# Kernel tuning notes

Measured on AMD Instinct MI355X. Metric: run time of the kernel, lower is better.

## Reference

```python
import jax, jax.numpy as jnp
import numpy as np

N_NODES = 100000
N_EDGES = 1600000
F_NODE = 32
F_EDGE = 32
HID = 64
N_TGT = 32


def setup_inputs() -> dict:
    key = jax.random.key(0)
    ks = jax.random.split(key, 12)
    x = jax.random.normal(ks[0], (N_NODES, F_NODE), dtype=jnp.float32)
    edge_index = jax.random.randint(ks[1], (2, N_EDGES), 0, N_NODES, dtype=jnp.int64)
    edge_attr = jax.random.normal(ks[2], (N_EDGES, F_EDGE), dtype=jnp.float32)
    u = jax.random.normal(ks[3], (1, 8), dtype=jnp.float32)
    batch = jnp.zeros((N_NODES,), dtype=jnp.int64)
    s1 = 1.0 / np.sqrt(F_NODE + F_EDGE)
    s2 = 1.0 / np.sqrt(HID)
    s3 = 1.0 / np.sqrt(HID + F_NODE)
    W1a = jax.random.uniform(ks[4], (F_NODE + F_EDGE, HID), jnp.float32, -s1, s1)
    b1a = jax.random.uniform(ks[5], (HID,), jnp.float32, -s1, s1)
    W1b = jax.random.uniform(ks[6], (HID, HID), jnp.float32, -s2, s2)
    b1b = jax.random.uniform(ks[7], (HID,), jnp.float32, -s2, s2)
    W2a = jax.random.uniform(ks[8], (HID + F_NODE, HID), jnp.float32, -s3, s3)
    b2a = jax.random.uniform(ks[9], (HID,), jnp.float32, -s3, s3)
    W2b = jax.random.uniform(ks[10], (HID, N_TGT), jnp.float32, -s2, s2)
    b2b = jax.random.uniform(ks[11], (N_TGT,), jnp.float32, -s2, s2)
    return {"x": x, "edge_index": edge_index, "edge_attr": edge_attr, "u": u,
            "batch": batch, "W1a": W1a, "b1a": b1a, "W1b": W1b, "b1b": b1b,
            "W2a": W2a, "b2a": b2a, "W2b": W2b, "b2b": b2b}


def reference(x, edge_index, edge_attr, u, batch,
              W1a, b1a, W1b, b1b, W2a, b2a, W2b, b2b):
    row, col = edge_index[0], edge_index[1]
    n = x.shape[0]
    # gather source node features and concat with edge features -> edge MLP
    m = jnp.concatenate([x[col], edge_attr], axis=1)           # [E, F_NODE+F_EDGE]
    m = jax.nn.relu(m @ W1a + b1a) @ W1b + b1b                  # [E, HID]
    # scatter-mean back to destination nodes (row)
    summed = jax.ops.segment_sum(m, row, num_segments=n)        # [N, HID]
    counts = jax.ops.segment_sum(jnp.ones((m.shape[0],), m.dtype), row, num_segments=n)
    agg = summed / jnp.maximum(counts, 1.0)[:, None]
    h = jnp.concatenate([x, agg], axis=1)                       # [N, HID+F_NODE]
    out = jax.nn.relu(h @ W2a + b2a) @ W2b + b2b                # [N, N_TGT]
    return out
```

## Files before the change

kernel.cpp:

```cpp
#include <hip/hip_runtime.h>

#define NN 100000
#define NE 1600000
#define NB ((NN + 255) / 256)
#define TPW 8

typedef unsigned int uint32;
typedef unsigned short ushort16;
typedef float f32x4 __attribute__((ext_vector_type(4)));
typedef short bf16x8 __attribute__((ext_vector_type(8)));

__device__ __forceinline__ float bflo(uint32 u) { return __uint_as_float(u << 16); }
__device__ __forceinline__ float bfhi(uint32 u) { return __uint_as_float(u & 0xffff0000u); }
__device__ __forceinline__ uint32 bfbits(float v) { return (__float_as_uint(v) + 0x8000u) >> 16; }
__device__ __forceinline__ uint32 pack2(float a, float b) { return bfbits(a) | (bfbits(b) << 16); }

__device__ __forceinline__ int sigma_ch(int c) {
    return (((c >> 2) & 3) << 4) + (((c >> 4) & 3) << 2) + (c & 3);
}

__global__ __launch_bounds__(256) void k_hist_rank(const int* __restrict__ ei, int* __restrict__ deg,
                                                   int* __restrict__ pos, int E) {
    int e = blockIdx.x * 256 + threadIdx.x;
    if (e < E) pos[e] = atomicAdd(&deg[ei[e]], 1);
}

__global__ __launch_bounds__(256) void k_hist(const int* __restrict__ ei, int* __restrict__ deg, int E) {
    int e = blockIdx.x * 256 + threadIdx.x;
    if (e < E) atomicAdd(&deg[ei[e]], 1);
}

__global__ __launch_bounds__(256) void k_scan1(const int* __restrict__ deg, int* __restrict__ offs,
                                               int* __restrict__ bsums, int n) {
    __shared__ int s[256];
    int tid = threadIdx.x;
    int i = blockIdx.x * 256 + tid;
    int v = (i < n) ? deg[i] : 0;
    int acc = v;
    s[tid] = acc;
    __syncthreads();
    #pragma unroll
    for (int off = 1; off < 256; off <<= 1) {
        int t = (tid >= off) ? s[tid - off] : 0;
        __syncthreads();
        acc += t;
        s[tid] = acc;
        __syncthreads();
    }
    if (i < n) offs[i] = acc - v;
    if (tid == 255) bsums[blockIdx.x] = acc;
}

__global__ __launch_bounds__(512) void k_scan2(int* __restrict__ bsums, int nb) {
    __shared__ int s[512];
    int tid = threadIdx.x;
    int v = (tid < nb) ? bsums[tid] : 0;
    int acc = v;
    s[tid] = acc;
    __syncthreads();
    #pragma unroll
    for (int off = 1; off < 512; off <<= 1) {
        int t = (tid >= off) ? s[tid - off] : 0;
        __syncthreads();
        acc += t;
        s[tid] = acc;
        __syncthreads();
    }
    bsums[tid] = acc - v;
}

__global__ __launch_bounds__(256) void k_pos(const int* __restrict__ ei, const int* __restrict__ offs,
                                             const int* __restrict__ bsums, int* __restrict__ pos, int E) {
    int e = blockIdx.x * 256 + threadIdx.x;
    if (e >= E) return;
    int r = ei[e];
    pos[e] += offs[r] + bsums[r >> 8];
}

__global__ __launch_bounds__(256) void k_prep(const float* __restrict__ W1b, const float* __restrict__ b1b,
                                              const float* __restrict__ W2a,
                                              float* __restrict__ Wc, float* __restrict__ bc, int perm) {
    int t = blockIdx.x * 256 + threadIdx.x;
    int r = t >> 6, c = t & 63;
    float a = 0.f;
    for (int k = 0; k < 64; ++k) a += W1b[r * 64 + k] * W2a[(32 + k) * 64 + c];
    int rs = perm ? sigma_ch(r) : r;
    Wc[rs * 64 + c] = a;
    if (t < 64) {
        float bacc = 0.f;
        for (int k = 0; k < 64; ++k) bacc += b1b[k] * W2a[(32 + k) * 64 + t];
        bc[t] = bacc;
    }
}

__global__ __launch_bounds__(256) void k_xa(const float* __restrict__ x, const float* __restrict__ W1a,
                                            const float* __restrict__ b1a, uint32* __restrict__ xa, int N) {
    __shared__ float sW[32 * 64];
    __shared__ float sb[64];
    for (int t = threadIdx.x; t < 32 * 64; t += 256) sW[t] = W1a[t];
    if (threadIdx.x < 64) sb[threadIdx.x] = b1a[threadIdx.x];
    __syncthreads();
    int i = blockIdx.x * 256 + threadIdx.x;
    if (i >= N) return;
    float h[64];
    #pragma unroll
    for (int j = 0; j < 64; ++j) h[j] = sb[j];
    const float4* xrow = (const float4*)(x + (size_t)i * 32);
    #pragma unroll
    for (int k4 = 0; k4 < 8; ++k4) {
        float4 v = xrow[k4];
        float vv[4] = {v.x, v.y, v.z, v.w};
        #pragma unroll
        for (int c = 0; c < 4; ++c) {
            const float4* wr = (const float4*)&sW[(k4 * 4 + c) * 64];
            float val = vv[c];
            #pragma unroll
            for (int j4 = 0; j4 < 16; ++j4) {
                float4 w = wr[j4];
                h[j4 * 4 + 0] += val * w.x; h[j4 * 4 + 1] += val * w.y;
                h[j4 * 4 + 2] += val * w.z; h[j4 * 4 + 3] += val * w.w;
            }
        }
    }
    uint32* xap = xa + (size_t)i * 32;
    #pragma unroll
    for (int q = 0; q < 4; ++q) {
        uint4 t0, t1;
        t0.x = pack2(h[0 * 16 + q * 4 + 0], h[0 * 16 + q * 4 + 1]);
        t0.y = pack2(h[0 * 16 + q * 4 + 2], h[0 * 16 + q * 4 + 3]);
        t0.z = pack2(h[1 * 16 + q * 4 + 0], h[1 * 16 + q * 4 + 1]);
        t0.w = pack2(h[1 * 16 + q * 4 + 2], h[1 * 16 + q * 4 + 3]);
        t1.x = pack2(h[2 * 16 + q * 4 + 0], h[2 * 16 + q * 4 + 1]);
        t1.y = pack2(h[2 * 16 + q * 4 + 2], h[2 * 16 + q * 4 + 3]);
        t1.z = pack2(h[3 * 16 + q * 4 + 0], h[3 * 16 + q * 4 + 1]);
        t1.w = pack2(h[3 * 16 + q * 4 + 2], h[3 * 16 + q * 4 + 3]);
        *(uint4*)(xap + q * 8) = t0;
        *(uint4*)(xap + q * 8 + 4) = t1;
    }
}

__global__ __launch_bounds__(256) void k_edge_mfma(
    const int* __restrict__ ei, const float* __restrict__ ea, const uint32* __restrict__ xa,
    const float* __restrict__ W1a, const int* __restrict__ pos, uint32* __restrict__ g)
{
    __shared__ ushort16 sWt[64 * 40];
    for (int idx = threadIdx.x; idx < 2048; idx += 256) {
        int ch = idx & 63, k = idx >> 6;
        sWt[ch * 40 + k] = (ushort16)bfbits(W1a[(32 + k) * 64 + ch]);
    }
    __syncthreads();

    int lane = threadIdx.x & 63;
    int wave = threadIdx.x >> 6;
    int en = lane & 15;
    int qq = lane >> 4;

    bf16x8 bfr[4];
    #pragma unroll
    for (int cc = 0; cc < 4; ++cc)
        bfr[cc] = *(const bf16x8*)&sWt[(cc * 16 + en) * 40 + qq * 8];

    int base = blockIdx.x * (64 * TPW) + wave * (16 * TPW);

    int e0 = base + en;
    int c0 = ei[NE + e0];
    int p0 = pos[e0];
    float4 f0a = *(const float4*)(ea + (size_t)e0 * 32 + qq * 8);
    float4 f0b = *(const float4*)(ea + (size_t)e0 * 32 + qq * 8 + 4);

    int e1 = base + 16 + en;
    int c1 = ei[NE + e1];
    int p1 = pos[e1];
    float4 f1a = *(const float4*)(ea + (size_t)e1 * 32 + qq * 8);
    float4 f1b = *(const float4*)(ea + (size_t)e1 * 32 + qq * 8 + 4);

    uint4 xv0a = *(const uint4*)(xa + (size_t)c0 * 32 + qq * 8);
    uint4 xv0b = *(const uint4*)(xa + (size_t)c0 * 32 + qq * 8 + 4);

    #pragma unroll 1
    for (int t = 0; t < TPW; ++t) {
        int e2 = base + (t + 2) * 16 + en;
        if (e2 > NE - 1) e2 = NE - 1;
        int c2 = ei[NE + e2];
        int p2 = pos[e2];
        float4 f2a = *(const float4*)(ea + (size_t)e2 * 32 + qq * 8);
        float4 f2b = *(const float4*)(ea + (size_t)e2 * 32 + qq * 8 + 4);
        uint4 xv1a = *(const uint4*)(xa + (size_t)c1 * 32 + qq * 8);
        uint4 xv1b = *(const uint4*)(xa + (size_t)c1 * 32 + qq * 8 + 4);

        union { uint4 u; bf16x8 v; } bf;
        bf.u.x = pack2(f0a.x, f0a.y);
        bf.u.y = pack2(f0a.z, f0a.w);
        bf.u.z = pack2(f0b.x, f0b.y);
        bf.u.w = pack2(f0b.z, f0b.w);

        f32x4 acc[4];
        acc[0] = (f32x4){bflo(xv0a.x), bfhi(xv0a.x), bflo(xv0a.y), bfhi(xv0a.y)};
        acc[1] = (f32x4){bflo(xv0a.z), bfhi(xv0a.z), bflo(xv0a.w), bfhi(xv0a.w)};
        acc[2] = (f32x4){bflo(xv0b.x), bfhi(xv0b.x), bflo(xv0b.y), bfhi(xv0b.y)};
        acc[3] = (f32x4){bflo(xv0b.z), bfhi(xv0b.z), bflo(xv0b.w), bfhi(xv0b.w)};

        #pragma unroll
        for (int cc = 0; cc < 4; ++cc)
            acc[cc] = __builtin_amdgcn_mfma_f32_16x16x32_bf16(bfr[cc], bf.v, acc[cc], 0, 0, 0);

        uint4 o0, o1;
        o0.x = pack2(fmaxf(acc[0][0], 0.f), fmaxf(acc[0][1], 0.f));
        o0.y = pack2(fmaxf(acc[0][2], 0.f), fmaxf(acc[0][3], 0.f));
        o0.z = pack2(fmaxf(acc[1][0], 0.f), fmaxf(acc[1][1], 0.f));
        o0.w = pack2(fmaxf(acc[1][2], 0.f), fmaxf(acc[1][3], 0.f));
        o1.x = pack2(fmaxf(acc[2][0], 0.f), fmaxf(acc[2][1], 0.f));
        o1.y = pack2(fmaxf(acc[2][2], 0.f), fmaxf(acc[2][3], 0.f));
        o1.z = pack2(fmaxf(acc[3][0], 0.f), fmaxf(acc[3][1], 0.f));
        o1.w = pack2(fmaxf(acc[3][2], 0.f), fmaxf(acc[3][3], 0.f));
        uint4* gp = (uint4*)(g + (size_t)p0 * 32 + qq * 8);
        gp[0] = o0;
        gp[1] = o1;

        c0 = c1; p0 = p1; f0a = f1a; f0b = f1b;
        xv0a = xv1a; xv0b = xv1b;
        c1 = c2; p1 = p2; f1a = f2a; f1b = f2b;
    }
}

__global__ __launch_bounds__(256) void k_seg_c(
    const int* __restrict__ deg, const int* __restrict__ offs, const int* __restrict__ bsums,
    const uint32* __restrict__ g, float* __restrict__ Sacc)
{
    int node = blockIdx.x * 4 + (threadIdx.x >> 6);
    if (node >= NN) return;
    int lane = threadIdx.x & 63;
    int quarter = lane >> 4;
    int wi = lane & 15;
    int d = deg[node];
    size_t start = (size_t)(offs[node] + bsums[node >> 8]);

    float4 S = {0.f, 0.f, 0.f, 0.f};
    int r = quarter;
    for (; r + 4 < d; r += 8) {
        uint2 u1 = *(const uint2*)(g + (start + r) * 32 + wi * 2);
        uint2 u2 = *(const uint2*)(g + (start + r + 4) * 32 + wi * 2);
        S.x += bflo(u1.x) + bflo(u2.x);
        S.y += bfhi(u1.x) + bfhi(u2.x);
        S.z += bflo(u1.y) + bflo(u2.y);
        S.w += bfhi(u1.y) + bfhi(u2.y);
    }
    if (r < d) {
        uint2 u = *(const uint2*)(g + (start + r) * 32 + wi * 2);
        S.x += bflo(u.x); S.y += bfhi(u.x); S.z += bflo(u.y); S.w += bfhi(u.y);
    }
    S.x += __shfl_xor(S.x, 16); S.y += __shfl_xor(S.y, 16);
    S.z += __shfl_xor(S.z, 16); S.w += __shfl_xor(S.w, 16);
    S.x += __shfl_xor(S.x, 32); S.y += __shfl_xor(S.y, 32);
    S.z += __shfl_xor(S.z, 32); S.w += __shfl_xor(S.w, 32);
    if (quarter == 0)
        *(float4*)(Sacc + (size_t)node * 64 + wi * 4) = make_float4(S.x, S.y, S.z, S.w);
}

__global__ __launch_bounds__(256) void k_edge_atom(
    const float* __restrict__ x, const int* __restrict__ ei, const float* __restrict__ ea,
    const float* __restrict__ W1a, const float* __restrict__ b1a,
    float* __restrict__ Sacc, int E)
{
    __shared__ float sWB[32 * 64];
    __shared__ float sWA[32 * 64];
    __shared__ float sb[64];
    for (int t = threadIdx.x; t < 32 * 64; t += 256) {
        sWB[t] = W1a[32 * 64 + t];
        sWA[t] = W1a[t];
    }
    if (threadIdx.x < 64) sb[threadIdx.x] = b1a[threadIdx.x];
    __syncthreads();
    int e = blockIdx.x * 256 + threadIdx.x;
    if (e >= E) return;
    int row = ei[e];
    int col = ei[NE + e];
    float h[64];
    #pragma unroll
    for (int j = 0; j < 64; ++j) h[j] = sb[j];
    const float4* xrow = (const float4*)(x + (size_t)col * 32);
    #pragma unroll
    for (int k4 = 0; k4 < 8; ++k4) {
        float4 v = xrow[k4];
        float vv[4] = {v.x, v.y, v.z, v.w};
        #pragma unroll
        for (int c = 0; c < 4; ++c) {
            float val = vv[c];
            const float4* wr = (const float4*)&sWA[(k4 * 4 + c) * 64];
            #pragma unroll
            for (int j4 = 0; j4 < 16; ++j4) {
                float4 w = wr[j4];
                h[j4 * 4 + 0] += val * w.x; h[j4 * 4 + 1] += val * w.y;
                h[j4 * 4 + 2] += val * w.z; h[j4 * 4 + 3] += val * w.w;
            }
        }
    }
    const float4* earow = (const float4*)(ea + (size_t)e * 32);
    #pragma unroll
    for (int k4 = 0; k4 < 8; ++k4) {
        float4 v = earow[k4];
        float vv[4] = {v.x, v.y, v.z, v.w};
        #pragma unroll
        for (int c = 0; c < 4; ++c) {
            float val = vv[c];
            const float4* wr = (const float4*)&sWB[(k4 * 4 + c) * 64];
            #pragma unroll
            for (int j4 = 0; j4 < 16; ++j4) {
                float4 w = wr[j4];
                h[j4 * 4 + 0] += val * w.x; h[j4 * 4 + 1] += val * w.y;
                h[j4 * 4 + 2] += val * w.z; h[j4 * 4 + 3] += val * w.w;
            }
        }
    }
    float* srow = Sacc + (size_t)row * 64;
    #pragma unroll
    for (int j = 0; j < 64; ++j) atomicAdd(&srow[j], fmaxf(h[j], 0.f));
}

__global__ __launch_bounds__(256) void k_node(
    const float* __restrict__ x, const float* __restrict__ Sacc, const int* __restrict__ deg,
    const float* __restrict__ Wc, const float* __restrict__ bc,
    const float* __restrict__ W2a, const float* __restrict__ b2a,
    const float* __restrict__ W2b, const float* __restrict__ b2b,
    float* __restrict__ out, int N)
{
    __shared__ float sWc[64 * 64];
    __shared__ float sW2ax[32 * 64];
    __shared__ float sW2b[64 * 32];
    __shared__ float sbc2[64];
    __shared__ float sb2[64];
    __shared__ float sb2b_[32];
    for (int t = threadIdx.x; t < 64 * 64; t += 256) sWc[t] = Wc[t];
    for (int t = threadIdx.x; t < 32 * 64; t += 256) sW2ax[t] = W2a[t];
    for (int t = threadIdx.x; t < 64 * 32; t += 256) sW2b[t] = W2b[t];
    if (threadIdx.x < 64) {
        sbc2[threadIdx.x] = bc[threadIdx.x] + b2a[threadIdx.x];
        sb2[threadIdx.x] = b2a[threadIdx.x];
    }
    if (threadIdx.x < 32) sb2b_[threadIdx.x] = b2b[threadIdx.x];
    __syncthreads();

    int i = blockIdx.x * 256 + threadIdx.x;
    if (i >= N) return;
    int d = deg[i];
    float inv = (d > 0) ? 1.f / (float)d : 0.f;

    float h2[64];
    #pragma unroll
    for (int j = 0; j < 64; ++j) h2[j] = (d > 0) ? sbc2[j] : sb2[j];

    const float4* sp = (const float4*)(Sacc + (size_t)i * 64);
    #pragma unroll 2
    for (int k4 = 0; k4 < 16; ++k4) {
        float4 v = sp[k4];
        float vv[4] = {v.x * inv, v.y * inv, v.z * inv, v.w * inv};
        #pragma unroll
        for (int c = 0; c < 4; ++c) {
            float val = vv[c];
            const float4* wr = (const float4*)&sWc[(k4 * 4 + c) * 64];
            #pragma unroll
            for (int j4 = 0; j4 < 16; ++j4) {
                float4 w = wr[j4];
                h2[j4 * 4 + 0] += val * w.x; h2[j4 * 4 + 1] += val * w.y;
                h2[j4 * 4 + 2] += val * w.z; h2[j4 * 4 + 3] += val * w.w;
            }
        }
    }
    const float4* xrow = (const float4*)(x + (size_t)i * 32);
    #pragma unroll 2
    for (int k4 = 0; k4 < 8; ++k4) {
        float4 v = xrow[k4];
        float vv[4] = {v.x, v.y, v.z, v.w};
        #pragma unroll
        for (int c = 0; c < 4; ++c) {
            float val = vv[c];
            const float4* wr = (const float4*)&sW2ax[(k4 * 4 + c) * 64];
            #pragma unroll
            for (int j4 = 0; j4 < 16; ++j4) {
                float4 w = wr[j4];
                h2[j4 * 4 + 0] += val * w.x; h2[j4 * 4 + 1] += val * w.y;
                h2[j4 * 4 + 2] += val * w.z; h2[j4 * 4 + 3] += val * w.w;
            }
        }
    }
    #pragma unroll
    for (int j = 0; j < 64; ++j) h2[j] = fmaxf(h2[j], 0.f);

    float o[32];
    #pragma unroll
    for (int j = 0; j < 32; ++j) o[j] = sb2b_[j];
    #pragma unroll
    for (int k = 0; k < 64; ++k) {
        float val = h2[k];
        const float4* wr = (const float4*)&sW2b[k * 32];
        #pragma unroll
        for (int j4 = 0; j4 < 8; ++j4) {
            float4 w = wr[j4];
            o[j4 * 4 + 0] += val * w.x; o[j4 * 4 + 1] += val * w.y;
            o[j4 * 4 + 2] += val * w.z; o[j4 * 4 + 3] += val * w.w;
        }
    }
    float4* orow = (float4*)(out + (size_t)i * 32);
    #pragma unroll
    for (int q = 0; q < 8; ++q)
        orow[q] = make_float4(o[q * 4], o[q * 4 + 1], o[q * 4 + 2], o[q * 4 + 3]);
}

extern "C" void kernel_launch(void* const* d_in, const int* in_sizes, int n_in,
                              void* d_out, int out_size, void* d_ws, size_t ws_size,
                              hipStream_t stream) {
    const float* x   = (const float*)d_in[0];
    const int*   ei  = (const int*)d_in[1];
    const float* ea  = (const float*)d_in[2];
    const float* W1a = (const float*)d_in[5];
    const float* b1a = (const float*)d_in[6];
    const float* W1b = (const float*)d_in[7];
    const float* b1b = (const float*)d_in[8];
    const float* W2a = (const float*)d_in[9];
    const float* b2a = (const float*)d_in[10];
    const float* W2b = (const float*)d_in[11];
    const float* b2b = (const float*)d_in[12];
    float* out = (float*)d_out;

    char* p = (char*)d_ws;
    int* deg        = (int*)p;        p += (size_t)NN * 4;
    int* offs       = (int*)p;        p += (size_t)NN * 4;
    int* bsums      = (int*)p;        p += 2048;
    float* Wc       = (float*)p;      p += 4096 * 4;
    float* bc       = (float*)p;      p += 64 * 4;
    int* pos        = (int*)p;        p += (size_t)NE * 4;
    uint32* xa      = (uint32*)p;     p += (size_t)NN * 64 * 2;
    float* Sacc     = (float*)p;      p += (size_t)NN * 64 * 4;
    size_t off_g    = (size_t)(p - (char*)d_ws);
    uint32* g       = (uint32*)p;

    dim3 blk(256);
    bool primary = (ws_size >= off_g + (size_t)NE * 128);

    if (primary) {
        hipMemsetAsync(deg, 0, (size_t)NN * 4, stream);
        hipLaunchKernelGGL(k_hist_rank, dim3((NE + 255) / 256), blk, 0, stream, ei, deg, pos, NE);
        hipLaunchKernelGGL(k_scan1, dim3(NB), blk, 0, stream, deg, offs, bsums, NN);
        hipLaunchKernelGGL(k_scan2, dim3(1), dim3(512), 0, stream, bsums, NB);
        hipLaunchKernelGGL(k_pos, dim3((NE + 255) / 256), blk, 0, stream, ei, offs, bsums, pos, NE);
        hipLaunchKernelGGL(k_prep, dim3(16), blk, 0, stream, W1b, b1b, W2a, Wc, bc, 1);
        hipLaunchKernelGGL(k_xa, dim3(NB), blk, 0, stream, x, W1a, b1a, xa, NN);
        hipLaunchKernelGGL(k_edge_mfma, dim3(NE / (64 * TPW)), blk, 0, stream, ei, ea, xa, W1a, pos, g);
        hipLaunchKernelGGL(k_seg_c, dim3((NN + 3) / 4), blk, 0, stream, deg, offs, bsums, g, Sacc);
        hipLaunchKernelGGL(k_node, dim3(NB), blk, 0, stream,
                           x, Sacc, deg, Wc, bc, W2a, b2a, W2b, b2b, out, NN);
    } else {
        hipMemsetAsync(deg, 0, (size_t)NN * 4, stream);
        hipMemsetAsync(Sacc, 0, (size_t)NN * 64 * 4, stream);
        hipLaunchKernelGGL(k_hist, dim3((NE + 255) / 256), blk, 0, stream, ei, deg, NE);
        hipLaunchKernelGGL(k_prep, dim3(16), blk, 0, stream, W1b, b1b, W2a, Wc, bc, 0);
        hipLaunchKernelGGL(k_edge_atom, dim3((NE + 255) / 256), blk, 0, stream,
                           x, ei, ea, W1a, b1a, Sacc, NE);
        hipLaunchKernelGGL(k_node, dim3(NB), blk, 0, stream,
                           x, Sacc, deg, Wc, bc, W2a, b2a, W2b, b2b, out, NN);
    }
}
```

Measured before the change: 331.9 us.

## Compute x-side edge projection with a second MFMA instead of precomputed xa table

Drops the per-node k_xa kernel that precomputed x@W1a+b1a into a 64-channel bf16 table. The edge kernel now gathers raw bf16 x rows (32 channels, half the bytes) and runs a second set of MFMAs against W1a's x rows, starting the accumulators from the bias. The W1a fragments are prepacked once by a merged prep kernel, so the per-block LDS staging and barrier go away. This halves the random gather traffic per edge at the cost of doubling MFMA work in the edge loop.

```diff
diff --git a/kernel.cpp b/kernel.cpp
--- a/kernel.cpp
+++ b/kernel.cpp
@@ -6,7 +6,6 @@
 #define TPW 8
 
 typedef unsigned int uint32;
-typedef unsigned short ushort16;
 typedef float f32x4 __attribute__((ext_vector_type(4)));
 typedef short bf16x8 __attribute__((ext_vector_type(8)));
 
@@ -77,132 +76,112 @@
     pos[e] += offs[r] + bsums[r >> 8];
 }
 
-__global__ __launch_bounds__(256) void k_prep(const float* __restrict__ W1b, const float* __restrict__ b1b,
-                                              const float* __restrict__ W2a,
-                                              float* __restrict__ Wc, float* __restrict__ bc, int perm) {
-    int t = blockIdx.x * 256 + threadIdx.x;
-    int r = t >> 6, c = t & 63;
-    float a = 0.f;
-    for (int k = 0; k < 64; ++k) a += W1b[r * 64 + k] * W2a[(32 + k) * 64 + c];
-    int rs = perm ? sigma_ch(r) : r;
-    Wc[rs * 64 + c] = a;
-    if (t < 64) {
-        float bacc = 0.f;
-        for (int k = 0; k < 64; ++k) bacc += b1b[k] * W2a[(32 + k) * 64 + t];
-        bc[t] = bacc;
-    }
-}
-
-__global__ __launch_bounds__(256) void k_xa(const float* __restrict__ x, const float* __restrict__ W1a,
-                                            const float* __restrict__ b1a, uint32* __restrict__ xa, int N) {
-    __shared__ float sW[32 * 64];
-    __shared__ float sb[64];
-    for (int t = threadIdx.x; t < 32 * 64; t += 256) sW[t] = W1a[t];
-    if (threadIdx.x < 64) sb[threadIdx.x] = b1a[threadIdx.x];
-    __syncthreads();
-    int i = blockIdx.x * 256 + threadIdx.x;
-    if (i >= N) return;
-    float h[64];
-    #pragma unroll
-    for (int j = 0; j < 64; ++j) h[j] = sb[j];
-    const float4* xrow = (const float4*)(x + (size_t)i * 32);
-    #pragma unroll
-    for (int k4 = 0; k4 < 8; ++k4) {
-        float4 v = xrow[k4];
-        float vv[4] = {v.x, v.y, v.z, v.w};
-        #pragma unroll
-        for (int c = 0; c < 4; ++c) {
-            const float4* wr = (const float4*)&sW[(k4 * 4 + c) * 64];
-            float val = vv[c];
+__global__ __launch_bounds__(256) void k_prep2(const float* __restrict__ W1b, const float* __restrict__ b1b,
+                                               const float* __restrict__ W2a, const float* __restrict__ W1a,
+                                               const float* __restrict__ x,
+                                               float* __restrict__ Wc, float* __restrict__ bc,
+                                               uint4* __restrict__ wpack, uint32* __restrict__ xbw,
+                                               int perm) {
+    int idx = blockIdx.x * 256 + threadIdx.x;
+    if (idx < 4096) {
+        int r = idx >> 6, c = idx & 63;
+        float a = 0.f;
+        for (int k = 0; k < 64; ++k) a += W1b[r * 64 + k] * W2a[(32 + k) * 64 + c];
+        int rs = perm ? sigma_ch(r) : r;
+        Wc[rs * 64 + c] = a;
+        if (idx < 64) {
+            float bacc = 0.f;
+            for (int k = 0; k < 64; ++k) bacc += b1b[k] * W2a[(32 + k) * 64 + idx];
+            bc[idx] = bacc;
+        }
+        if (idx < 512) {
+            int table = idx >> 8;
+            int cc = (idx >> 6) & 3;
+            int lane = idx & 63;
+            int qq = lane >> 4, en = lane & 15;
+            int ch = cc * 16 + en;
+            uint32 w[4];
             #pragma unroll
-            for (int j4 = 0; j4 < 16; ++j4) {
-                float4 w = wr[j4];
-                h[j4 * 4 + 0] += val * w.x; h[j4 * 4 + 1] += val * w.y;
-                h[j4 * 4 + 2] += val * w.z; h[j4 * 4 + 3] += val * w.w;
+            for (int j = 0; j < 4; ++j) {
+                int row0 = (table ? 0 : 32) + qq * 8 + j * 2;
+                w[j] = pack2(W1a[row0 * 64 + ch], W1a[(row0 + 1) * 64 + ch]);
             }
-        }
-    }
-    uint32* xap = xa + (size_t)i * 32;
-    #pragma unroll
-    for (int q = 0; q < 4; ++q) {
-        uint4 t0, t1;
-        t0.x = pack2(h[0 * 16 + q * 4 + 0], h[0 * 16 + q * 4 + 1]);
-        t0.y = pack2(h[0 * 16 + q * 4 + 2], h[0 * 16 + q * 4 + 3]);
-        t0.z = pack2(h[1 * 16 + q * 4 + 0], h[1 * 16 + q * 4 + 1]);
-        t0.w = pack2(h[1 * 16 + q * 4 + 2], h[1 * 16 + q * 4 + 3]);
-        t1.x = pack2(h[2 * 16 + q * 4 + 0], h[2 * 16 + q * 4 + 1]);
-        t1.y = pack2(h[2 * 16 + q * 4 + 2], h[2 * 16 + q * 4 + 3]);
-        t1.z = pack2(h[3 * 16 + q * 4 + 0], h[3 * 16 + q * 4 + 1]);
-        t1.w = pack2(h[3 * 16 + q * 4 + 2], h[3 * 16 + q * 4 + 3]);
-        *(uint4*)(xap + q * 8) = t0;
-        *(uint4*)(xap + q * 8 + 4) = t1;
+            wpack[idx] = make_uint4(w[0], w[1], w[2], w[3]);
+        }
+    }
+    int xi = idx - 4096;
+    if (xi >= 0 && xi < NN * 16) {
+        float2 v = *(const float2*)(x + (size_t)2 * xi);
+        xbw[xi] = pack2(v.x, v.y);
     }
 }
 
 __global__ __launch_bounds__(256) void k_edge_mfma(
-    const int* __restrict__ ei, const float* __restrict__ ea, const uint32* __restrict__ xa,
-    const float* __restrict__ W1a, const int* __restrict__ pos, uint32* __restrict__ g)
+    const int* __restrict__ ei, const float* __restrict__ ea, const uint32* __restrict__ xbw,
+    const uint4* __restrict__ wpack, const float* __restrict__ b1a,
+    const int* __restrict__ pos, uint32* __restrict__ g)
 {
-    __shared__ ushort16 sWt[64 * 40];
-    for (int idx = threadIdx.x; idx < 2048; idx += 256) {
-        int ch = idx & 63, k = idx >> 6;
-        sWt[ch * 40 + k] = (ushort16)bfbits(W1a[(32 + k) * 64 + ch]);
-    }
-    __syncthreads();
-
     int lane = threadIdx.x & 63;
     int wave = threadIdx.x >> 6;
     int en = lane & 15;
     int qq = lane >> 4;
 
-    bf16x8 bfr[4];
-    #pragma unroll
-    for (int cc = 0; cc < 4; ++cc)
-        bfr[cc] = *(const bf16x8*)&sWt[(cc * 16 + en) * 40 + qq * 8];
+    union U { uint4 u; bf16x8 v; };
+    U wB[4], wA[4];
+    #pragma unroll
+    for (int cc = 0; cc < 4; ++cc) {
+        wB[cc].u = wpack[cc * 64 + lane];
+        wA[cc].u = wpack[256 + cc * 64 + lane];
+    }
+    f32x4 binit[4];
+    #pragma unroll
+    for (int cc = 0; cc < 4; ++cc) {
+        float4 b = *(const float4*)(b1a + cc * 16 + qq * 4);
+        binit[cc] = (f32x4){b.x, b.y, b.z, b.w};
+    }
 
     int base = blockIdx.x * (64 * TPW) + wave * (16 * TPW);
 
     int e0 = base + en;
+    int p0 = pos[e0];
     int c0 = ei[NE + e0];
-    int p0 = pos[e0];
     float4 f0a = *(const float4*)(ea + (size_t)e0 * 32 + qq * 8);
     float4 f0b = *(const float4*)(ea + (size_t)e0 * 32 + qq * 8 + 4);
 
     int e1 = base + 16 + en;
+    int p1 = pos[e1];
     int c1 = ei[NE + e1];
-    int p1 = pos[e1];
     float4 f1a = *(const float4*)(ea + (size_t)e1 * 32 + qq * 8);
     float4 f1b = *(const float4*)(ea + (size_t)e1 * 32 + qq * 8 + 4);
 
-    uint4 xv0a = *(const uint4*)(xa + (size_t)c0 * 32 + qq * 8);
-    uint4 xv0b = *(const uint4*)(xa + (size_t)c0 * 32 + qq * 8 + 4);
+    uint4 xv0 = *(const uint4*)(xbw + (size_t)c0 * 16 + qq * 4);
 
     #pragma unroll 1
     for (int t = 0; t < TPW; ++t) {
         int e2 = base + (t + 2) * 16 + en;
         if (e2 > NE - 1) e2 = NE - 1;
+        int p2 = pos[e2];
         int c2 = ei[NE + e2];
-        int p2 = pos[e2];
         float4 f2a = *(const float4*)(ea + (size_t)e2 * 32 + qq * 8);
         float4 f2b = *(const float4*)(ea + (size_t)e2 * 32 + qq * 8 + 4);
-        uint4 xv1a = *(const uint4*)(xa + (size_t)c1 * 32 + qq * 8);
-        uint4 xv1b = *(const uint4*)(xa + (size_t)c1 * 32 + qq * 8 + 4);
-
-        union { uint4 u; bf16x8 v; } bf;
-        bf.u.x = pack2(f0a.x, f0a.y);
-        bf.u.y = pack2(f0a.z, f0a.w);
-        bf.u.z = pack2(f0b.x, f0b.y);
-        bf.u.w = pack2(f0b.z, f0b.w);
+        uint4 xv1 = *(const uint4*)(xbw + (size_t)c1 * 16 + qq * 4);
+
+        U bea, bx;
+        bea.u.x = pack2(f0a.x, f0a.y);
+        bea.u.y = pack2(f0a.z, f0a.w);
+        bea.u.z = pack2(f0b.x, f0b.y);
+        bea.u.w = pack2(f0b.z, f0b.w);
+        bx.u = xv0;
 
         f32x4 acc[4];
-        acc[0] = (f32x4){bflo(xv0a.x), bfhi(xv0a.x), bflo(xv0a.y), bfhi(xv0a.y)};
-        acc[1] = (f32x4){bflo(xv0a.z), bfhi(xv0a.z), bflo(xv0a.w), bfhi(xv0a.w)};
-        acc[2] = (f32x4){bflo(xv0b.x), bfhi(xv0b.x), bflo(xv0b.y), bfhi(xv0b.y)};
-        acc[3] = (f32x4){bflo(xv0b.z), bfhi(xv0b.z), bflo(xv0b.w), bfhi(xv0b.w)};
-
+        #pragma unroll
+        for (int cc = 0; cc < 4; ++cc) acc[cc] = binit[cc];
         #pragma unroll
         for (int cc = 0; cc < 4; ++cc)
-            acc[cc] = __builtin_amdgcn_mfma_f32_16x16x32_bf16(bfr[cc], bf.v, acc[cc], 0, 0, 0);
+            acc[cc] = __builtin_amdgcn_mfma_f32_16x16x32_bf16(wB[cc].v, bea.v, acc[cc], 0, 0, 0);
+        #pragma unroll
+        for (int cc = 0; cc < 4; ++cc)
+            acc[cc] = __builtin_amdgcn_mfma_f32_16x16x32_bf16(wA[cc].v, bx.v, acc[cc], 0, 0, 0);
 
         uint4 o0, o1;
         o0.x = pack2(fmaxf(acc[0][0], 0.f), fmaxf(acc[0][1], 0.f));
@@ -217,9 +196,8 @@
         gp[0] = o0;
         gp[1] = o1;
 
-        c0 = c1; p0 = p1; f0a = f1a; f0b = f1b;
-        xv0a = xv1a; xv0b = xv1b;
-        c1 = c2; p1 = p2; f1a = f2a; f1b = f2b;
+        p0 = p1; f0a = f1a; f0b = f1b; xv0 = xv1;
+        p1 = p2; c1 = c2; f1a = f2a; f1b = f2b;
     }
 }
 
@@ -428,24 +406,27 @@
     int* bsums      = (int*)p;        p += 2048;
     float* Wc       = (float*)p;      p += 4096 * 4;
     float* bc       = (float*)p;      p += 64 * 4;
+    uint4* wpack    = (uint4*)p;      p += 512 * 16;
     int* pos        = (int*)p;        p += (size_t)NE * 4;
-    uint32* xa      = (uint32*)p;     p += (size_t)NN * 64 * 2;
+    uint32* xbw     = (uint32*)p;     p += (size_t)NN * 16 * 4;
     float* Sacc     = (float*)p;      p += (size_t)NN * 64 * 4;
     size_t off_g    = (size_t)(p - (char*)d_ws);
     uint32* g       = (uint32*)p;
+    size_t need     = off_g + (size_t)NE * 128;
 
     dim3 blk(256);
-    bool primary = (ws_size >= off_g + (size_t)NE * 128);
-
-    if (primary) {
+    int prep_grid = (4096 + NN * 16 + 255) / 256;
+
+    if (ws_size >= need) {
         hipMemsetAsync(deg, 0, (size_t)NN * 4, stream);
         hipLaunchKernelGGL(k_hist_rank, dim3((NE + 255) / 256), blk, 0, stream, ei, deg, pos, NE);
         hipLaunchKernelGGL(k_scan1, dim3(NB), blk, 0, stream, deg, offs, bsums, NN);
         hipLaunchKernelGGL(k_scan2, dim3(1), dim3(512), 0, stream, bsums, NB);
         hipLaunchKernelGGL(k_pos, dim3((NE + 255) / 256), blk, 0, stream, ei, offs, bsums, pos, NE);
-        hipLaunchKernelGGL(k_prep, dim3(16), blk, 0, stream, W1b, b1b, W2a, Wc, bc, 1);
-        hipLaunchKernelGGL(k_xa, dim3(NB), blk, 0, stream, x, W1a, b1a, xa, NN);
-        hipLaunchKernelGGL(k_edge_mfma, dim3(NE / (64 * TPW)), blk, 0, stream, ei, ea, xa, W1a, pos, g);
+        hipLaunchKernelGGL(k_prep2, dim3(prep_grid), blk, 0, stream,
+                           W1b, b1b, W2a, W1a, x, Wc, bc, wpack, xbw, 1);
+        hipLaunchKernelGGL(k_edge_mfma, dim3(NE / (64 * TPW)), blk, 0, stream,
+                           ei, ea, xbw, wpack, b1a, pos, g);
         hipLaunchKernelGGL(k_seg_c, dim3((NN + 3) / 4), blk, 0, stream, deg, offs, bsums, g, Sacc);
         hipLaunchKernelGGL(k_node, dim3(NB), blk, 0, stream,
                            x, Sacc, deg, Wc, bc, W2a, b2a, W2b, b2b, out, NN);
@@ -453,7 +434,8 @@
         hipMemsetAsync(deg, 0, (size_t)NN * 4, stream);
         hipMemsetAsync(Sacc, 0, (size_t)NN * 64 * 4, stream);
         hipLaunchKernelGGL(k_hist, dim3((NE + 255) / 256), blk, 0, stream, ei, deg, NE);
-        hipLaunchKernelGGL(k_prep, dim3(16), blk, 0, stream, W1b, b1b, W2a, Wc, bc, 0);
+        hipLaunchKernelGGL(k_prep2, dim3(prep_grid), blk, 0, stream,
+                           W1b, b1b, W2a, W1a, x, Wc, bc, wpack, xbw, 0);
         hipLaunchKernelGGL(k_edge_atom, dim3((NE + 255) / 256), blk, 0, stream,
                            x, ei, ea, W1a, b1a, Sacc, NE);
         hipLaunchKernelGGL(k_node, dim3(NB), blk, 0, stream,
```

Result: faster. 306.1 us (-7.8%).
